# Performance work log

Measured on AMD Instinct MI355X. Metric: run time of the kernel, lower is better.

The kernel has to match this reference:

```python
import jax, jax.numpy as jnp
import numpy as np
from jax import lax

B, C, H, G = 128, 512, 14, 20  # batch, channels, feature-map size, num branches

# landmark indices for (point1, point2) of the 10 regions, and y-offset coefficients (x ruler)
_I1 = jnp.array([21, 18, 19, 41, 38, 49, 48, 51, 61, 56])
_I2 = jnp.array([22, 25, 24, 46, 43, 53, 54, 57, 63, 58])
_COEF = jnp.array([-0.5, -1.0 / 3.0, 1.0 / 3.0, 1.0, 0.0, 0.0, 0.0, 0.0, 0.0, 0.5], jnp.float32)


def process_landmarks(y):
    # y: [B,68,2] (x,y) pixel coords -> region_array [B,10,4] = (x1,y1,x2,y2)/16
    xl, yl = y[:, :, 0], y[:, :, 1]
    ruler = jnp.abs(xl[:, 39] - xl[:, 42])            # [B]
    off = ruler[:, None] * _COEF[None, :]             # [B,10]
    region = jnp.stack([xl[:, _I1], yl[:, _I1] + off, xl[:, _I2], yl[:, _I2] + off], axis=-1)
    return region / 16.0


def _crop(xi, cyi, cxi):
    # xi: [C,H,W]; 3x3 window centered at (cyi, cxi)
    z = jnp.asarray(0, cyi.dtype)
    return lax.dynamic_slice(xi, (z, cyi - 1, cxi - 1), (C, 3, 3))


def setup_inputs() -> dict:
    key = jax.random.key(0)
    ks = jax.random.split(key, 4)
    x = jax.random.normal(ks[0], (B, C, H, H), jnp.float32)
    y = jax.random.uniform(ks[1], (B, 68, 2), jnp.float32) * 224.0
    conv_w = jax.random.normal(ks[2], (G * C, C, 3, 3), jnp.float32) * 0.02  # grouped OIHW
    conv_b = jnp.zeros((G * C,), jnp.float32)
    fc_w = jax.random.normal(ks[3], (G, C * 36, 150), jnp.float32) * 0.01
    fc_b = jnp.zeros((G, 150), jnp.float32)
    return {"x": x, "y": y, "conv_w": conv_w, "conv_b": conv_b, "fc_w": fc_w, "fc_b": fc_b}


def reference(x, y, conv_w, conv_b, fc_w, fc_b):
    bsz = x.shape[0]
    pos = jnp.clip(process_landmarks(y).astype(jnp.int32), 1, 12)   # [B,10,4]
    cx = pos[:, :, jnp.array([0, 2])].reshape(bsz, G)               # [B,20] cols
    cy = pos[:, :, jnp.array([1, 3])].reshape(bsz, G)               # [B,20] rows
    crops = jax.vmap(jax.vmap(_crop, in_axes=(None, 0, 0)), in_axes=(0, 0, 0))(x, cy, cx)  # [B,20,C,3,3]
    new_input = crops.reshape(bsz, G * C, 3, 3)
    up = jax.image.resize(new_input, (bsz, G * C, 6, 6), method='bilinear')  # half-pixel, matches torch align_corners=False
    conv = lax.conv_general_dilated(up, conv_w, (1, 1), ((1, 1), (1, 1)),
                                    feature_group_count=G,
                                    dimension_numbers=('NCHW', 'OIHW', 'NCHW'))
    conv = jax.nn.relu(conv + conv_b[None, :, None, None])          # [B, G*C, 6, 6]
    feat = conv.reshape(bsz, G, C * 36)
    fc = jax.nn.relu(jnp.einsum('bgi,gio->bgo', feat, fc_w) + fc_b[None])  # [B,G,150]
    return fc.reshape(bsz, G * 150)
```

## Files before the change

kernel.cpp:

```cpp
#include <hip/hip_runtime.h>
#include <stdint.h>

#define B_  128
#define C_  512
#define G_  20
#define K2  4608
#define FCK 18432

typedef unsigned short u16;
typedef unsigned int   u32;
typedef __attribute__((ext_vector_type(8))) short  short8;
typedef __attribute__((ext_vector_type(4))) short  short4v;
typedef __attribute__((ext_vector_type(4))) float  float4v;

__device__ __forceinline__ u16 f2bf(float f) {
  u32 u = __builtin_bit_cast(u32, f);
  u = (u + 0x7fffu + ((u >> 16) & 1u)) >> 16;
  return (u16)u;
}

__device__ __forceinline__ float bf2f(u16 h) {
  u32 u = ((u32)h) << 16;
  return __builtin_bit_cast(float, u);
}

__device__ __forceinline__ void load_lds16(const void* g, void* l) {
  __builtin_amdgcn_global_load_lds(
      (const __attribute__((address_space(1))) void*)(uintptr_t)g,
      (__attribute__((address_space(3))) void*)(uint32_t)(uintptr_t)l,
      16, 0, 0);
}

#define BAR() __builtin_amdgcn_s_barrier()

__global__ void k_pos(const float* __restrict__ y, int* __restrict__ cx, int* __restrict__ cy) {
  int b = blockIdx.x * blockDim.x + threadIdx.x;
  if (b >= B_) return;
  const int   I1[10] = {21,18,19,41,38,49,48,51,61,56};
  const int   I2[10] = {22,25,24,46,43,53,54,57,63,58};
  const float CF[10] = {-0.5f, -1.0f/3.0f, 1.0f/3.0f, 1.0f, 0.f,0.f,0.f,0.f,0.f, 0.5f};
  const float* yb = y + b * 136;
  float ruler = fabsf(yb[2*39] - yb[2*42]);
  for (int j = 0; j < 10; ++j) {
    float off = ruler * CF[j];
    float vx1 = yb[2*I1[j]];
    float vy1 = yb[2*I1[j]+1] + off;
    float vx2 = yb[2*I2[j]];
    float vy2 = yb[2*I2[j]+1] + off;
    int px1 = (int)(vx1 * 0.0625f); px1 = min(max(px1,1),12);
    int py1 = (int)(vy1 * 0.0625f); py1 = min(max(py1,1),12);
    int px2 = (int)(vx2 * 0.0625f); px2 = min(max(px2,1),12);
    int py2 = (int)(vy2 * 0.0625f); py2 = min(max(py2,1),12);
    cx[b*20 + 2*j]   = px1;  cx[b*20 + 2*j+1] = px2;
    cy[b*20 + 2*j]   = py1;  cy[b*20 + 2*j+1] = py2;
  }
}

__global__ void __launch_bounds__(256) k_pre1(const float* __restrict__ w, u16* __restrict__ wb,
                                              const float* __restrict__ x, u16* __restrict__ xT) {
  __shared__ __align__(16) char smraw[4 * 4608 * 2];
  int tid = threadIdx.x;
  if (blockIdx.x < 2560) {
    u16* lds = (u16*)smraw;
    int ob = blockIdx.x * 4;
    const float4* in4 = (const float4*)(w + (size_t)ob * 4608);
    #pragma unroll
    for (int r = 0; r < 18; ++r) {
      int fi = r * 256 + tid;
      float4 v = in4[fi];
      u16 q[4] = { f2bf(v.x), f2bf(v.y), f2bf(v.z), f2bf(v.w) };
      *(short4v*)&lds[fi * 4] = *(short4v*)q;
    }
    __syncthreads();
    #pragma unroll
    for (int r = 0; r < 9; ++r) {
      int wi = r * 256 + tid;
      int ci0 = (wi & 63) * 8;
      int t   = (wi >> 6) % 9;
      int o   = wi / 576;
      u16 vals[8];
      #pragma unroll
      for (int j = 0; j < 8; ++j) vals[j] = lds[o * 4608 + (ci0 + j) * 9 + t];
      *(short8*)(wb + ((size_t)(ob + o)) * K2 + t * 512 + ci0) = *(short8*)vals;
    }
  } else {
    u16* lds = (u16*)smraw;
    int cid = blockIdx.x - 2560;
    int b = cid >> 3, cic = (cid & 7) * 64;
    const float* src = x + ((size_t)b * C_ + cic) * 196;
    #pragma unroll
    for (int it = 0; it < 49; ++it) {
      int idx = it * 256 + tid;
      int ci = idx / 196, p = idx - ci * 196;
      lds[ci * 197 + p] = f2bf(src[(size_t)ci * 196 + p]);
    }
    __syncthreads();
    u16* dst = xT + (size_t)b * 196 * C_ + cic;
    #pragma unroll
    for (int it = 0; it < 7; ++it) {
      int idx = it * 256 + tid;
      if (idx < 1568) {
        int p = idx >> 3, c8 = (idx & 7) * 8;
        u16 vals[8];
        #pragma unroll
        for (int j = 0; j < 8; ++j) vals[j] = lds[(c8 + j) * 197 + p];
        *(short8*)(dst + (size_t)p * C_ + c8) = *(short8*)vals;
      }
    }
  }
}

__global__ void __launch_bounds__(256) k_pre2(const u16* __restrict__ xT,
                                              const int* __restrict__ cx,
                                              const int* __restrict__ cy,
                                              u16* __restrict__ up3) {
  __shared__ float crop[3][3][C_];
  int bg = blockIdx.x;
  int b = bg / 20, g = bg % 20;
  int X = cx[bg] - 1, Y = cy[bg] - 1;
  int tid = threadIdx.x;
  const u16* xb = xT + (size_t)b * 196 * C_;
  #pragma unroll
  for (int it = 0; it < 3; ++it) {
    int idx = it * 256 + tid;
    if (idx < 576) {
      int pos = idx >> 6;
      int r = pos / 3, s = pos - r * 3;
      int c8 = (idx & 63) * 8;
      short8 v = *(const short8*)(xb + (size_t)((Y + r) * 14 + X + s) * C_ + c8);
      #pragma unroll
      for (int j = 0; j < 8; ++j) crop[r][s][c8 + j] = bf2f((u16)v[j]);
    }
  }
  __syncthreads();
  const int   R0[6] = {0,0,0,1,1,1};
  const float WA[6] = {1.f, .75f, .25f, .75f, .25f, 0.f};
  u16* dstbase = up3 + ((size_t)g*B_ + b) * 64 * C_;
  for (int it = 0; it < 16; ++it) {
    int cidx = it*256 + tid;
    int pp = cidx >> 6;
    int c8 = (cidx & 63) * 8;
    int ph = pp >> 3, pw = pp & 7;
    u16 outv[8];
    if (ph == 0 || ph == 7 || pw == 0 || pw == 7) {
      #pragma unroll
      for (int j = 0; j < 8; ++j) outv[j] = 0;
    } else {
      int oh = ph - 1, ow = pw - 1;
      int r0 = R0[oh]; float wy0 = WA[oh], wy1 = 1.f - WA[oh];
      int s0 = R0[ow]; float wx0 = WA[ow], wx1 = 1.f - WA[ow];
      #pragma unroll
      for (int j = 0; j < 8; ++j) {
        int ci = c8 + j;
        float v = wy0*(wx0*crop[r0][s0][ci]   + wx1*crop[r0][s0+1][ci])
                + wy1*(wx0*crop[r0+1][s0][ci] + wx1*crop[r0+1][s0+1][ci]);
        outv[j] = f2bf(v);
      }
    }
    *(short8*)(dstbase + (size_t)pp*C_ + c8) = *(short8*)outv;
  }
}

__global__ void __launch_bounds__(512, 2) k_conv(const u16* __restrict__ wb,
                                                 const u16* __restrict__ up3,
                                                 const float* __restrict__ conv_b,
                                                 u16* __restrict__ feat) {
  __shared__ __align__(16) u16 As[2 * 256 * 64];
  __shared__ __align__(16) u16 Bs[2 * 256 * 64];
  int bid = blockIdx.x;
  int tid = threadIdx.x;
  int lid = (bid & 7) * 90 + (bid >> 3);
  int mt = lid & 1;
  int nt = (lid >> 1) % 18;
  int g  = lid / 36;
  int lane = tid & 63;
  int w = tid >> 6;
  int wr = w >> 2, wc = w & 3;
  int l15 = lane & 15, l4 = lane >> 4;

  int rl0 = tid >> 3, sl0 = tid & 7;
  const u16* srcA0 = wb + (size_t)(g*512 + mt*256 + rl0) * K2 + (sl0 ^ (rl0 & 7)) * 8;
  const u16* srcB[2][2];
  #pragma unroll
  for (int h = 0; h < 2; ++h)
    #pragma unroll
    for (int j = 0; j < 2; ++j) {
      int rl = j * 64 + rl0;
      int n  = nt * 256 + h * 128 + rl;
      unsigned bb = (unsigned)n / 36u;
      unsigned pix = (unsigned)n % 36u;
      int pixA = (int)(pix / 6u) * 8 + (int)(pix % 6u);
      srcB[h][j] = up3 + (((size_t)g*B_ + bb)*64 + pixA) * C_ + (sl0 ^ (rl0 & 7)) * 8;
    }

  auto stageA = [&](int st, int h) {
    if (st >= 72) return;
    int db = st & 1;
    size_t ko = (size_t)st * 64;
    #pragma unroll
    for (int j = 0; j < 2; ++j)
      load_lds16(srcA0 + (size_t)(h*128 + j*64) * K2 + ko,
                 (char*)As + db*32768 + h*16384 + (j*512 + tid)*16);
  };
  auto stageB = [&](int st, int h) {
    if (st >= 72) return;
    int db = st & 1;
    int t9 = st >> 3;
    size_t ko = (size_t)((t9/3)*8 + (t9%3)) * C_ + (size_t)(st & 7) * 64;
    #pragma unroll
    for (int j = 0; j < 2; ++j)
      load_lds16(srcB[h][j] + ko,
                 (char*)Bs + db*32768 + h*16384 + (j*512 + tid)*16);
  };

  auto ldfrag = [&](const char* base, int row, int kb) -> short8 {
    int cb = (kb*64 + l4*16) ^ ((row & 7) << 4);
    return *(const short8*)(base + row*128 + cb);
  };

  float4v acc[8][4];
  #pragma unroll
  for (int mi = 0; mi < 8; ++mi)
    #pragma unroll
    for (int nj = 0; nj < 4; ++nj) acc[mi][nj] = (float4v){0.f,0.f,0.f,0.f};

  stageB(0,0); stageB(0,1); stageA(0,0); stageA(0,1);
  stageB(1,0); stageB(1,1); stageA(1,0); stageA(1,1);
  asm volatile("s_waitcnt vmcnt(8)" ::: "memory");
  BAR();

  short8 aF[4][2], b01[2][2], b23[2][2];

#define LDA_HALF(BASE, MH)                                        \
  _Pragma("unroll") for (int mi = 0; mi < 4; ++mi)                \
    _Pragma("unroll") for (int kb = 0; kb < 2; ++kb)              \
      aF[mi][kb] = ldfrag(BASE, wr*128 + ((MH)*4 + mi)*16 + l15, kb);
#define LDB_HALF(BASE, NH, DST)                                   \
  _Pragma("unroll") for (int nj = 0; nj < 2; ++nj)                \
    _Pragma("unroll") for (int kb = 0; kb < 2; ++kb)              \
      DST[nj][kb] = ldfrag(BASE, wc*64 + ((NH)*2 + nj)*16 + l15, kb);
#define MFMA_QUAD(BF, QM, QN)                                     \
  __builtin_amdgcn_s_setprio(1);                                  \
  _Pragma("unroll") for (int kb = 0; kb < 2; ++kb)                \
    _Pragma("unroll") for (int mi = 0; mi < 4; ++mi)              \
      _Pragma("unroll") for (int nj = 0; nj < 2; ++nj)            \
        acc[(QM)*4+mi][(QN)*2+nj] = __builtin_amdgcn_mfma_f32_16x16x32_bf16( \
            aF[mi][kb], BF[nj][kb], acc[(QM)*4+mi][(QN)*2+nj], 0, 0, 0);     \
  __builtin_amdgcn_s_setprio(0);

  for (int it = 0; it < 36; ++it) {
    int t0 = 2 * it;
    const char* A0 = (const char*)As;
    const char* B0 = (const char*)Bs;
    const char* A1 = (const char*)As + 32768;
    const char* B1 = (const char*)Bs + 32768;
    LDA_HALF(A0, 0); LDB_HALF(B0, 0, b01);
    BAR(); MFMA_QUAD(b01, 0, 0);
    LDB_HALF(B0, 1, b23);
    BAR(); MFMA_QUAD(b23, 0, 1);
    LDA_HALF(A0, 1);
    stageB(t0 + 2, 0);
    BAR(); MFMA_QUAD(b01, 1, 0);
    stageB(t0 + 2, 1); stageA(t0 + 2, 0);
    BAR(); MFMA_QUAD(b23, 1, 1);
    if (it < 35) { asm volatile("s_waitcnt vmcnt(6)" ::: "memory"); }
    else         { asm volatile("s_waitcnt vmcnt(0)" ::: "memory"); }
    BAR();
    LDA_HALF(A1, 0); LDB_HALF(B1, 0, b01);
    stageA(t0 + 2, 1);
    BAR(); MFMA_QUAD(b01, 0, 0);
    LDB_HALF(B1, 1, b23);
    BAR(); MFMA_QUAD(b23, 0, 1);
    LDA_HALF(A1, 1);
    stageB(t0 + 3, 0);
    BAR(); MFMA_QUAD(b01, 1, 0);
    stageB(t0 + 3, 1); stageA(t0 + 3, 0);
    BAR();
    stageA(t0 + 3, 1);
    MFMA_QUAD(b23, 1, 1);
    asm volatile("s_waitcnt vmcnt(8)" ::: "memory");
    BAR();
  }
#undef LDA_HALF
#undef LDB_HALF
#undef MFMA_QUAD

  float bias[8][4];
  #pragma unroll
  for (int mi = 0; mi < 8; ++mi)
    #pragma unroll
    for (int r = 0; r < 4; ++r)
      bias[mi][r] = conv_b[g*512 + mt*256 + wr*128 + mi*16 + l4*4 + r];
  #pragma unroll
  for (int nj = 0; nj < 4; ++nj) {
    int n = nt*256 + wc*64 + nj*16 + l15;
    unsigned bb = (unsigned)n / 36u;
    unsigned pix = (unsigned)n % 36u;
    size_t base = ((size_t)g*B_ + bb)*FCK + (size_t)pix*512;
    #pragma unroll
    for (int mi = 0; mi < 8; ++mi) {
      int co0 = mt*256 + wr*128 + mi*16 + l4*4;
      u16 q[4];
      #pragma unroll
      for (int r = 0; r < 4; ++r)
        q[r] = f2bf(fmaxf(acc[mi][nj][r] + bias[mi][r], 0.f));
      *(short4v*)(feat + base + co0) = *(short4v*)q;
    }
  }
}

__global__ void __launch_bounds__(256) k_fc(const u16* __restrict__ feat,
                                            const float* __restrict__ fw,
                                            float* __restrict__ accum) {
  __shared__ __align__(16) u16 As[128*64];
  __shared__ __align__(16) u16 Bs[160*64];
  int sp = blockIdx.x;
  int g  = blockIdx.y;
  int tid = threadIdx.x;
  int lane = tid & 63, w = tid >> 6;
  int wr = w >> 1, wc = w & 1;
  int rl = lane >> 3, s = lane & 7;
  int l15 = lane & 15, l4 = lane >> 4;

  const u16* gA[4]; u16* lA[4];
  #pragma unroll
  for (int i = 0; i < 4; ++i) {
    int r = w*32 + i*8 + rl;
    int c = s ^ (r & 7);
    gA[i] = feat + ((size_t)g*B_ + r)*FCK + c*8;
    lA[i] = (u16*)As + (w*32 + i*8) * 64;
  }

  float4v acc[4][5];
  #pragma unroll
  for (int mi = 0; mi < 4; ++mi)
    #pragma unroll
    for (int nj = 0; nj < 5; ++nj) acc[mi][nj] = (float4v){0.f,0.f,0.f,0.f};

  int kbase = sp * 576;
  for (int stp = 0; stp < 9; ++stp) {
    int i0 = kbase + stp * 64;
    int pix = i0 >> 9;
    int cobase = i0 & 511;
    __syncthreads();
    #pragma unroll
    for (int i = 0; i < 4; ++i) load_lds16(gA[i] + i0, lA[i]);
    #pragma unroll
    for (int bit = 0; bit < 5; ++bit) {
      int idx = bit * 256 + tid;
      int il8 = idx / 160;
      int o   = idx - il8 * 160;
      u16 vals[8];
      if (o < 150) {
        const float* src = fw + ((size_t)g * FCK + (size_t)(cobase + il8 * 8) * 36 + pix) * 150 + o;
        #pragma unroll
        for (int j = 0; j < 8; ++j) vals[j] = f2bf(src[(size_t)j * 5400]);
      } else {
        #pragma unroll
        for (int j = 0; j < 8; ++j) vals[j] = 0;
      }
      *(short8*)((char*)Bs + o * 128 + ((il8 ^ (o & 7)) * 16)) = *(short8*)vals;
    }
    __syncthreads();

    short8 a[4][2], bf[5][2];
    #pragma unroll
    for (int kb = 0; kb < 2; ++kb) {
      #pragma unroll
      for (int mi = 0; mi < 4; ++mi) {
        int row = wr*64 + mi*16 + l15;
        int cb  = (kb*64 + l4*16) ^ ((row & 7) << 4);
        a[mi][kb] = *(const short8*)((const char*)As + row*128 + cb);
      }
      #pragma unroll
      for (int nj = 0; nj < 5; ++nj) {
        int row = wc*80 + nj*16 + l15;
        int cb  = (kb*64 + l4*16) ^ ((row & 7) << 4);
        bf[nj][kb] = *(const short8*)((const char*)Bs + row*128 + cb);
      }
    }
    #pragma unroll
    for (int kb = 0; kb < 2; ++kb)
      #pragma unroll
      for (int mi = 0; mi < 4; ++mi)
        #pragma unroll
        for (int nj = 0; nj < 5; ++nj)
          acc[mi][nj] = __builtin_amdgcn_mfma_f32_16x16x32_bf16(
              a[mi][kb], bf[nj][kb], acc[mi][nj], 0, 0, 0);
  }

  #pragma unroll
  for (int mi = 0; mi < 4; ++mi)
    #pragma unroll
    for (int r = 0; r < 4; ++r) {
      int brow = wr*64 + mi*16 + l4*4 + r;
      #pragma unroll
      for (int nj = 0; nj < 5; ++nj) {
        int o = wc*80 + nj*16 + l15;
        atomicAdd(&accum[((size_t)brow*20 + g)*160 + o], acc[mi][nj][r]);
      }
    }
}

__global__ void k_final(const float* __restrict__ accum, const float* __restrict__ fcb,
                        float* __restrict__ out) {
  int idx = blockIdx.x * 256 + threadIdx.x;
  if (idx >= B_*3000) return;
  unsigned b = (unsigned)idx / 3000u;
  unsigned rem = (unsigned)idx % 3000u;
  unsigned g = rem / 150u, o = rem % 150u;
  out[idx] = fmaxf(accum[((size_t)b*20 + g)*160 + o] + fcb[g*150 + o], 0.f);
}

extern "C" void kernel_launch(void* const* d_in, const int* in_sizes, int n_in,
                              void* d_out, int out_size, void* d_ws, size_t ws_size,
                              hipStream_t stream) {
  const float* x      = (const float*)d_in[0];
  const float* y      = (const float*)d_in[1];
  const float* conv_w = (const float*)d_in[2];
  const float* conv_b = (const float*)d_in[3];
  const float* fc_w   = (const float*)d_in[4];
  const float* fc_b   = (const float*)d_in[5];
  float* out = (float*)d_out;

  char* ws = (char*)d_ws;
  size_t off = 0;
  u16* Wb   = (u16*)(ws + off); off += (size_t)10240 * K2 * 2;
  u16* up3  = (u16*)(ws + off); off += (size_t)G_ * B_ * 64 * C_ * 2;
  u16* feat = (u16*)(ws + off); off += (size_t)G_ * B_ * FCK * 2;
  u16* xT   = (u16*)(ws + off); off += (size_t)B_ * 196 * C_ * 2;
  float* accum = (float*)(ws + off); off += (size_t)B_ * G_ * 160 * 4;
  int* cx = (int*)(ws + off); off += B_ * G_ * 4;
  int* cy = (int*)(ws + off); off += B_ * G_ * 4;

  k_pos<<<1, 128, 0, stream>>>(y, cx, cy);
  hipMemsetAsync(accum, 0, (size_t)B_ * G_ * 160 * 4, stream);
  k_pre1<<<3584, 256, 0, stream>>>(conv_w, Wb, x, xT);
  k_pre2<<<B_*G_, 256, 0, stream>>>(xT, cx, cy, up3);
  k_conv<<<720, 512, 0, stream>>>(Wb, up3, conv_b, feat);
  k_fc<<<dim3(32, 20), 256, 0, stream>>>(feat, fc_w, accum);
  k_final<<<(B_*3000 + 255)/256, 256, 0, stream>>>(accum, fc_b, out);
}
```

Before: 559.5 us.

## Double-buffer register fragments across conv GEMM main loop phases

Restructures the conv GEMM main loop so that LDS fragment loads for the next quadrant go into alternate register sets (Aa/Ab, Bc/Bd) while MFMAs consume the current set. The first fragments are preloaded before the loop. Global-to-LDS staging is reordered and now waits with vmcnt(0) at mid-phase. The intent is to hide LDS read latency behind MFMA issue. In exchange it uses more VGPRs, which may lower occupancy, and the stricter vmcnt(0) waits may expose global load latency.

After: 625.7 us. 1.12x slower.

```diff
diff --git a/kernel.cpp b/kernel.cpp
--- a/kernel.cpp
+++ b/kernel.cpp
@@ -224,66 +224,64 @@
     #pragma unroll
     for (int nj = 0; nj < 4; ++nj) acc[mi][nj] = (float4v){0.f,0.f,0.f,0.f};
 
-  stageB(0,0); stageB(0,1); stageA(0,0); stageA(0,1);
-  stageB(1,0); stageB(1,1); stageA(1,0); stageA(1,1);
-  asm volatile("s_waitcnt vmcnt(8)" ::: "memory");
-  BAR();
-
-  short8 aF[4][2], b01[2][2], b23[2][2];
-
-#define LDA_HALF(BASE, MH)                                        \
+  const char* A0 = (const char*)As;
+  const char* B0 = (const char*)Bs;
+  const char* A1 = (const char*)As + 32768;
+  const char* B1 = (const char*)Bs + 32768;
+
+  short8 Aa[4][2], Ab[4][2], Bc[2][2], Bd[2][2];
+
+#define LDA_SET(DST, BASE, MH)                                    \
   _Pragma("unroll") for (int mi = 0; mi < 4; ++mi)                \
     _Pragma("unroll") for (int kb = 0; kb < 2; ++kb)              \
-      aF[mi][kb] = ldfrag(BASE, wr*128 + ((MH)*4 + mi)*16 + l15, kb);
-#define LDB_HALF(BASE, NH, DST)                                   \
+      DST[mi][kb] = ldfrag(BASE, wr*128 + ((MH)*4 + mi)*16 + l15, kb);
+#define LDB_SET(DST, BASE, NH)                                    \
   _Pragma("unroll") for (int nj = 0; nj < 2; ++nj)                \
     _Pragma("unroll") for (int kb = 0; kb < 2; ++kb)              \
       DST[nj][kb] = ldfrag(BASE, wc*64 + ((NH)*2 + nj)*16 + l15, kb);
-#define MFMA_QUAD(BF, QM, QN)                                     \
+#define MQ(ASET, BSET, QM, QN)                                    \
   __builtin_amdgcn_s_setprio(1);                                  \
   _Pragma("unroll") for (int kb = 0; kb < 2; ++kb)                \
     _Pragma("unroll") for (int mi = 0; mi < 4; ++mi)              \
       _Pragma("unroll") for (int nj = 0; nj < 2; ++nj)            \
         acc[(QM)*4+mi][(QN)*2+nj] = __builtin_amdgcn_mfma_f32_16x16x32_bf16( \
-            aF[mi][kb], BF[nj][kb], acc[(QM)*4+mi][(QN)*2+nj], 0, 0, 0);     \
+            ASET[mi][kb], BSET[nj][kb], acc[(QM)*4+mi][(QN)*2+nj], 0, 0, 0); \
   __builtin_amdgcn_s_setprio(0);
+
+  stageB(0,0); stageA(0,0); stageB(0,1); stageA(0,1);
+  stageB(1,0); stageA(1,0); stageB(1,1); stageA(1,1);
+  asm volatile("s_waitcnt vmcnt(8)" ::: "memory");
+  BAR();
+  LDA_SET(Aa, A0, 0); LDB_SET(Bc, B0, 0);
 
   for (int it = 0; it < 36; ++it) {
     int t0 = 2 * it;
-    const char* A0 = (const char*)As;
-    const char* B0 = (const char*)Bs;
-    const char* A1 = (const char*)As + 32768;
-    const char* B1 = (const char*)Bs + 32768;
-    LDA_HALF(A0, 0); LDB_HALF(B0, 0, b01);
-    BAR(); MFMA_QUAD(b01, 0, 0);
-    LDB_HALF(B0, 1, b23);
-    BAR(); MFMA_QUAD(b23, 0, 1);
-    LDA_HALF(A0, 1);
-    stageB(t0 + 2, 0);
-    BAR(); MFMA_QUAD(b01, 1, 0);
-    stageB(t0 + 2, 1); stageA(t0 + 2, 0);
-    BAR(); MFMA_QUAD(b23, 1, 1);
-    if (it < 35) { asm volatile("s_waitcnt vmcnt(6)" ::: "memory"); }
-    else         { asm volatile("s_waitcnt vmcnt(0)" ::: "memory"); }
-    BAR();
-    LDA_HALF(A1, 0); LDB_HALF(B1, 0, b01);
-    stageA(t0 + 2, 1);
-    BAR(); MFMA_QUAD(b01, 0, 0);
-    LDB_HALF(B1, 1, b23);
-    BAR(); MFMA_QUAD(b23, 0, 1);
-    LDA_HALF(A1, 1);
-    stageB(t0 + 3, 0);
-    BAR(); MFMA_QUAD(b01, 1, 0);
-    stageB(t0 + 3, 1); stageA(t0 + 3, 0);
-    BAR();
-    stageA(t0 + 3, 1);
-    MFMA_QUAD(b23, 1, 1);
-    asm volatile("s_waitcnt vmcnt(8)" ::: "memory");
-    BAR();
-  }
-#undef LDA_HALF
-#undef LDB_HALF
-#undef MFMA_QUAD
+    LDA_SET(Ab, A0, 1);
+    BAR(); MQ(Aa, Bc, 0, 0);
+    LDB_SET(Bd, B0, 1);
+    asm volatile("s_waitcnt vmcnt(0)" ::: "memory");
+    BAR(); MQ(Aa, Bd, 0, 1);
+    LDA_SET(Aa, A1, 0);
+    stageB(t0 + 2, 0); stageA(t0 + 2, 0);
+    BAR(); MQ(Ab, Bc, 1, 0);
+    LDB_SET(Bc, B1, 0);
+    stageB(t0 + 2, 1); stageA(t0 + 2, 1);
+    BAR(); MQ(Ab, Bd, 1, 1);
+    LDA_SET(Ab, A1, 1);
+    BAR(); MQ(Aa, Bc, 0, 0);
+    LDB_SET(Bd, B1, 1);
+    asm volatile("s_waitcnt vmcnt(0)" ::: "memory");
+    BAR(); MQ(Aa, Bd, 0, 1);
+    LDA_SET(Aa, A0, 0);
+    stageB(t0 + 3, 0); stageA(t0 + 3, 0);
+    BAR(); MQ(Ab, Bc, 1, 0);
+    LDB_SET(Bc, B0, 0);
+    stageB(t0 + 3, 1); stageA(t0 + 3, 1);
+    BAR(); MQ(Ab, Bd, 1, 1);
+  }
+#undef LDA_SET
+#undef LDB_SET
+#undef MQ
 
   float bias[8][4];
   #pragma unroll
```
